# Optimization experiments

Measured on AMD Instinct MI355X. Metric: run time of the kernel, lower is better.

## Reference

```python
import jax, jax.numpy as jnp
import numpy as np

N_SIGMA = 1
K_MAX = 8          # max number of non-zero instance ids
FG_W = 1.0         # foreground_weight
W_INST, W_VAR, W_SEED = 1.0, 10.0, 1.0


def _lovasz_hinge_flat(logits, labels_f):
    # logits, labels_f: [P] flat; standard Lovasz hinge (descending-error sort)
    signs = 2.0 * labels_f - 1.0
    errors = 1.0 - logits * signs
    perm = jnp.argsort(-errors)
    errors_sorted = errors[perm]
    gt_sorted = labels_f[perm]
    gts = gt_sorted.sum()
    cum = jnp.cumsum(gt_sorted)
    intersection = gts - cum
    union = gts + jnp.cumsum(1.0 - gt_sorted)
    jaccard = 1.0 - intersection / union
    grad = jnp.concatenate([jaccard[:1], jaccard[1:] - jaccard[:-1]])
    return jnp.sum(jax.nn.relu(errors_sorted) * jax.lax.stop_gradient(grad))


def _spatial_emb_loss(prediction, instances, labels):
    B, C, H, W = prediction.shape
    inst = instances[:, 0]  # [B,H,W]
    # coordinate buffer: linspace over the full 1024x2048 grid, then sliced
    xm = jnp.linspace(0.0, 2.0, 2048)[:W]
    ym = jnp.linspace(0.0, 1.0, 1024)[:H]
    xym = jnp.stack([jnp.broadcast_to(xm[None, :], (H, W)),
                     jnp.broadcast_to(ym[:, None], (H, W))])  # [2,H,W]
    ids = jnp.arange(1, K_MAX + 1)

    def per_image(pred, ins, lab):
        spatial_emb = jnp.tanh(pred[0:2]) + xym            # [2,H,W]
        sigma = pred[2]                                     # [H,W] (n_sigma=1)
        seed = jax.nn.sigmoid(pred[3])                      # [H,W]
        bg = (lab == 0)
        seed_loss_bg = jnp.sum(jnp.where(bg, seed ** 2, 0.0))
        masks = (ins[None] == ids[:, None, None])           # [K,H,W]
        mf = masks.astype(pred.dtype)
        counts = mf.sum((1, 2))                             # [K]
        present = counts > 0
        cnt = jnp.maximum(counts, 1.0)
        # to_center=True: center = mean of xym over instance pixels
        center = jnp.einsum('chw,khw->kc', xym, mf) / cnt[:, None]   # [K,2]
        s_mean = jnp.einsum('hw,khw->k', sigma, mf) / cnt            # [K]
        var_k = jnp.einsum('khw,khw->k',
                           (sigma[None] - jax.lax.stop_gradient(s_mean)[:, None, None]) ** 2,
                           mf) / cnt
        s_exp = jnp.exp(10.0 * s_mean)                                # [K]
        d2 = jnp.sum((spatial_emb[None] - center[:, :, None, None]) ** 2, axis=1)  # [K,H,W]
        dist = jnp.exp(-s_exp[:, None, None] * d2)                    # [K,H,W]
        lov = jax.vmap(_lovasz_hinge_flat)(2.0 * dist.reshape(K_MAX, -1) - 1.0,
                                           mf.reshape(K_MAX, -1))     # [K]
        seed_fg = jnp.einsum('khw,khw->k',
                             (seed[None] - jax.lax.stop_gradient(dist)) ** 2, mf)
        objf = jnp.maximum(present.sum().astype(pred.dtype), 1.0)
        inst_loss = jnp.where(present, lov, 0.0).sum() / objf
        var_loss = jnp.where(present, var_k, 0.0).sum() / objf
        seed_loss = (seed_loss_bg + FG_W * jnp.where(present, seed_fg, 0.0).sum()) / (H * W)
        return W_INST * inst_loss + W_VAR * var_loss + W_SEED * seed_loss

    per = jax.vmap(per_image)(prediction, inst, labels)
    return per.mean() + 0.0 * prediction.sum()


def setup_inputs() -> dict:
    key = jax.random.key(0)
    k1, k2, k3 = jax.random.split(key, 3)
    B, H, W = 4, 512, 1024
    prediction = jax.random.normal(k1, (B, 2 + N_SIGMA + 1, H, W), dtype=jnp.float32)
    instances = jax.random.randint(k2, (B, 1, H, W), 0, K_MAX + 1, dtype=jnp.int32)
    labels = jax.random.randint(k3, (B, H, W), 0, 2, dtype=jnp.int32)
    return {"prediction": prediction, "instances": instances, "labels": labels}


def reference(prediction, instances, labels):
    return _spatial_emb_loss(prediction, instances, labels)
```

## Files before the change

kernel.cpp:

```cpp
#include <hip/hip_runtime.h>
#include <math.h>

namespace {
constexpr int B_ = 4, K_ = 8, W_ = 1024;
constexpr int N_ = 512 * 1024;
constexpr int M_ = 128;
constexpr int MP_ = M_ + 1;
constexpr int BK_ = B_ * K_;
constexpr int KM_ = K_ * M_;

constexpr int HB_ = 512;
constexpr int HBPB_ = HB_ / B_;
constexpr int HCH_ = N_ / HBPB_;
constexpr int SB_ = 1024;
constexpr int SBPB_ = SB_ / B_;
constexpr int SCH_ = N_ / SBPB_;
constexpr int NSTAT = 41;
constexpr int NHC_ = 4;

constexpr size_t GHN_OFF_W  = 0;
constexpr size_t GHF_OFF_W  = GHN_OFF_W + B_ * KM_;
constexpr size_t SFG_OFF_W  = GHF_OFF_W + B_ * KM_;
constexpr size_t PSTAT_OFF_W = SFG_OFF_W + (size_t)BK_ * HBPB_;
constexpr size_t WSF_OFF_W  = PSTAT_OFF_W + (size_t)B_ * NSTAT * SBPB_;

constexpr int CNT_OFF  = 0;
constexpr int OBJF_OFF = 32;
}

__device__ __forceinline__ float fsigmoid_(float x) { return 1.0f / (1.0f + __expf(-x)); }
__device__ __forceinline__ float ftanh_(float x) { return 1.0f - 2.0f / (__expf(2.0f * x) + 1.0f); }

__global__ __launch_bounds__(256) void stats_kernel(const float* __restrict__ pred,
                                                    const int* __restrict__ inst,
                                                    const int* __restrict__ lab,
                                                    float* __restrict__ pstat,
                                                    unsigned int* __restrict__ gh,
                                                    float* __restrict__ out) {
    int tid = threadIdx.x;
    if (blockIdx.x < 32) {
        gh[blockIdx.x * 256 + tid] = 0u;
        if (blockIdx.x == 0 && tid == 0) out[0] = 0.0f;
    }
    int b = blockIdx.x >> 8;
    int blk = blockIdx.x & (SBPB_ - 1);
    int pix0 = blk * SCH_;

    const float* sigp = pred + ((long long)b * 4 + 2) * N_;
    const float* p3p  = pred + ((long long)b * 4 + 3) * N_;
    const int*   insp = inst + (long long)b * N_;
    const int*   labp = lab  + (long long)b * N_;

    float acc[NSTAT];
#pragma unroll
    for (int i = 0; i < NSTAT; i++) acc[i] = 0.0f;

#pragma unroll
    for (int it = 0; it < SCH_ / (256 * 4); it++) {
        int base = pix0 + (it * 256 + tid) * 4;
        float4 sg = *(const float4*)(sigp + base);
        float4 q3 = *(const float4*)(p3p + base);
        int4 in4 = *(const int4*)(insp + base);
        int4 lb4 = *(const int4*)(labp + base);
        float ss[4] = {sg.x, sg.y, sg.z, sg.w};
        float qq[4] = {q3.x, q3.y, q3.z, q3.w};
        int ii[4] = {in4.x, in4.y, in4.z, in4.w};
        int ll[4] = {lb4.x, lb4.y, lb4.z, lb4.w};
#pragma unroll
        for (int j = 0; j < 4; j++) {
            int pix = base + j;
            float xm = (float)(pix & (W_ - 1)) * (2.0f / 2047.0f);
            float ym = (float)(pix >> 10) * (1.0f / 1023.0f);
            float seed = fsigmoid_(qq[j]);
            if (ll[j] == 0) acc[40] += seed * seed;
            float s = ss[j];
#pragma unroll
            for (int k = 0; k < K_; k++) {
                float m = (ii[j] == k + 1) ? 1.0f : 0.0f;
                acc[k * 5]     += m;
                acc[k * 5 + 1] += m * xm;
                acc[k * 5 + 2] += m * ym;
                acc[k * 5 + 3] += m * s;
                acc[k * 5 + 4] += m * s * s;
            }
        }
    }
#pragma unroll
    for (int i = 0; i < NSTAT; i++) {
        float v = acc[i];
#pragma unroll
        for (int off = 32; off; off >>= 1) v += __shfl_down(v, off, 64);
        acc[i] = v;
    }
    __shared__ float xw[4][NSTAT];
    if ((tid & 63) == 0) {
        int w = tid >> 6;
#pragma unroll
        for (int i = 0; i < NSTAT; i++) xw[w][i] = acc[i];
    }
    __syncthreads();
    if (tid < NSTAT)
        pstat[((b * NSTAT + tid) << 8) + blk] =
            xw[0][tid] + xw[1][tid] + xw[2][tid] + xw[3][tid];
}

__global__ __launch_bounds__(256) void hist_kernel(const float* __restrict__ pred,
                                                   const int* __restrict__ inst,
                                                   const float* __restrict__ pstat,
                                                   float* __restrict__ wsf,
                                                   unsigned int* __restrict__ ghn,
                                                   unsigned int* __restrict__ ghf,
                                                   float* __restrict__ sfgpart,
                                                   float* __restrict__ out) {
    __shared__ float sq[NSTAT][4];
    __shared__ float ssum[NSTAT];
    __shared__ float prm[K_][4];
    __shared__ float svar[K_];
    __shared__ int spres[K_];
    __shared__ unsigned int hsh[NHC_][K_ * MP_];
    __shared__ float xfg[4][K_];

    int tid = threadIdx.x;
    int b = blockIdx.x >> 7;
    int blk = blockIdx.x & (HBPB_ - 1);
    int pix0 = blk * HCH_;

    if (tid < NSTAT * 4) {
        int row = tid >> 2, q = tid & 3;
        const float4* p = (const float4*)(pstat + ((size_t)(b * NSTAT + row) << 8)) + q * 16;
        float4 a = {0, 0, 0, 0};
#pragma unroll
        for (int j = 0; j < 16; j++) {
            float4 v = p[j];
            a.x += v.x; a.y += v.y; a.z += v.z; a.w += v.w;
        }
        sq[row][q] = (a.x + a.y) + (a.z + a.w);
    }
    for (int i = tid; i < NHC_ * K_ * MP_; i += 256) (&hsh[0][0])[i] = 0u;
    __syncthreads();
    if (tid < NSTAT) ssum[tid] = (sq[tid][0] + sq[tid][1]) + (sq[tid][2] + sq[tid][3]);
    __syncthreads();
    if (tid < K_) {
        float counts = ssum[tid * 5];
        float cnt = fmaxf(counts, 1.0f);
        float smean = ssum[tid * 5 + 3] / cnt;
        prm[tid][0] = ssum[tid * 5 + 1] / cnt;
        prm[tid][1] = ssum[tid * 5 + 2] / cnt;
        prm[tid][2] = expf(10.0f * smean);
        prm[tid][3] = counts;
        if (blk == 0) {
            svar[tid] = (counts > 0.0f) ? ssum[tid * 5 + 4] / cnt - smean * smean : 0.0f;
            spres[tid] = counts > 0.0f ? 1 : 0;
            wsf[CNT_OFF + b * K_ + tid] = counts;
        }
    }
    __syncthreads();
    if (blk == 0 && tid == 0) {
        float np = 0.0f, vl = 0.0f;
#pragma unroll
        for (int k = 0; k < K_; k++) { np += (float)spres[k]; vl += svar[k]; }
        float objf = fmaxf(np, 1.0f);
        wsf[OBJF_OFF + b] = objf;
        atomicAdd(out, (10.0f * vl / objf + ssum[40] / (float)N_) * (1.0f / (float)B_));
    }

    float cx[K_], cy[K_], sxp[K_];
    bool prs[K_];
#pragma unroll
    for (int k = 0; k < K_; k++) {
        cx[k] = prm[k][0]; cy[k] = prm[k][1]; sxp[k] = prm[k][2];
        prs[k] = prm[k][3] > 0.0f;
    }
    unsigned int* hpriv = &hsh[tid & 3][0];

    const float* p0p = pred + ((long long)b * 4) * N_;
    const float* p1p = p0p + N_;
    const float* p3p = p0p + 3LL * N_;
    const int* insp = inst + (long long)b * N_;

    float sfg[K_];
#pragma unroll
    for (int k = 0; k < K_; k++) sfg[k] = 0.0f;

#pragma unroll
    for (int it = 0; it < HCH_ / (256 * 4); it++) {
        int base = pix0 + (it * 256 + tid) * 4;
        float4 a0 = *(const float4*)(p0p + base);
        float4 a1 = *(const float4*)(p1p + base);
        float4 a3 = *(const float4*)(p3p + base);
        int4 in4 = *(const int4*)(insp + base);
        float v0[4] = {a0.x, a0.y, a0.z, a0.w};
        float v1[4] = {a1.x, a1.y, a1.z, a1.w};
        float v3[4] = {a3.x, a3.y, a3.z, a3.w};
        int ii[4] = {in4.x, in4.y, in4.z, in4.w};
#pragma unroll
        for (int j = 0; j < 4; j++) {
            int pix = base + j;
            float sex = ftanh_(v0[j]) + (float)(pix & (W_ - 1)) * (2.0f / 2047.0f);
            float sey = ftanh_(v1[j]) + (float)(pix >> 10) * (1.0f / 1023.0f);
            float seed = fsigmoid_(v3[j]);
            int ins = ii[j];
#pragma unroll
            for (int k = 0; k < K_; k++) {
                if (prs[k]) {
                    float dx = sex - cx[k];
                    float dy = sey - cy[k];
                    float dist = __expf(-sxp[k] * (dx * dx + dy * dy));
                    bool fg = (ins == k + 1);
                    int ib = (int)fminf(128.0f * dist, 127.0f);
                    int bin = fg ? 127 - ib : ib;
                    atomicAdd(hpriv + (k * MP_ + bin), fg ? 0x10001u : 1u);
                    if (fg) { float d = seed - dist; sfg[k] += d * d; }
                }
            }
        }
    }
    __syncthreads();

    for (int i = tid; i < KM_; i += 256) {
        int r = (i >> 7) * MP_ + (i & (M_ - 1));
        unsigned int s = hsh[0][r] + hsh[1][r] + hsh[2][r] + hsh[3][r];
        if (s) {
            atomicAdd(&ghn[b * KM_ + i], s & 0xffffu);
            unsigned int hi = s >> 16;
            if (hi) atomicAdd(&ghf[b * KM_ + i], hi);
        }
    }

#pragma unroll
    for (int k = 0; k < K_; k++) {
        float v = sfg[k];
#pragma unroll
        for (int off = 32; off; off >>= 1) v += __shfl_down(v, off, 64);
        sfg[k] = v;
    }
    if ((tid & 63) == 0) {
        int w = tid >> 6;
#pragma unroll
        for (int k = 0; k < K_; k++) xfg[w][k] = sfg[k];
    }
    __syncthreads();
    if (tid < K_)
        sfgpart[(size_t)(b * K_ + tid) * HBPB_ + blk] =
            xfg[0][tid] + xfg[1][tid] + xfg[2][tid] + xfg[3][tid];
}

__global__ __launch_bounds__(256) void lovasz_kernel(const unsigned int* __restrict__ ghn,
                                                     const unsigned int* __restrict__ ghf,
                                                     const float* __restrict__ sfgpart,
                                                     const float* __restrict__ wsf,
                                                     float* __restrict__ out) {
    int bk = blockIdx.x;
    int b = bk >> 3, k = bk & 7;
    int tid = threadIdx.x;

    __shared__ unsigned int sn[M_], sf[M_];
    __shared__ float lovp;
    __shared__ float xs[2];
    if (tid < M_) {
        sn[tid] = ghn[(size_t)b * KM_ + k * M_ + tid];
        sf[tid] = ghf[(size_t)b * KM_ + k * M_ + tid];
    }
    __syncthreads();

    float pcnt = wsf[CNT_OFF + bk];
    float pp = fmaxf(pcnt, 1.0f);

    if (tid < 64) {
        uint2 vn = *(const uint2*)&sn[2 * tid];
        uint2 vf = *(const uint2*)&sf[2 * tid];
        unsigned long long p0 = ((unsigned long long)vn.x << 32) | (unsigned long long)vf.x;
        unsigned long long p1 = ((unsigned long long)vn.y << 32) | (unsigned long long)vf.y;
        unsigned long long T = p0 + p1;
#pragma unroll
        for (int off = 1; off < 64; off <<= 1) {
            unsigned long long t = __shfl_down(T, off, 64);
            if (tid + off < 64) T += t;
        }
        unsigned long long S0 = T;
        unsigned long long S1 = T - p0;
        float acc;
        {
            unsigned int R = (unsigned int)(S0 >> 32), F = (unsigned int)S0;
            float J = (R == 0) ? 0.0f : (1.0f - (pp - (float)F) / (pp + (float)(R - F)));
            acc = (tid == 0 ? 0.5f : 1.0f) * J;
        }
        {
            unsigned int R = (unsigned int)(S1 >> 32), F = (unsigned int)S1;
            float J = (R == 0) ? 0.0f : (1.0f - (pp - (float)F) / (pp + (float)(R - F)));
            acc += J;
        }
#pragma unroll
        for (int off = 32; off; off >>= 1) acc += __shfl_down(acc, off, 64);
        if (tid == 0) lovp = acc;
    } else if (tid >= 128) {
        float sv = sfgpart[(size_t)bk * HBPB_ + (tid - 128)];
#pragma unroll
        for (int off = 32; off; off >>= 1) sv += __shfl_down(sv, off, 64);
        if ((tid & 63) == 0) xs[(tid - 128) >> 6] = sv;
    }
    __syncthreads();

    if (tid == 0 && pcnt > 0.0f) {
        float lov = lovp * (2.0f / (float)M_);
        float sfgt = xs[0] + xs[1];
        float objf = wsf[OBJF_OFF + b];
        atomicAdd(out, (lov / objf + sfgt / (float)N_) * (1.0f / (float)B_));
    }
}

extern "C" void kernel_launch(void* const* d_in, const int* in_sizes, int n_in,
                              void* d_out, int out_size, void* d_ws, size_t ws_size,
                              hipStream_t stream) {
    const float* pred = (const float*)d_in[0];
    const int* inst = (const int*)d_in[1];
    const int* lab = (const int*)d_in[2];
    float* out = (float*)d_out;

    unsigned int* gh = (unsigned int*)d_ws;
    unsigned int* ghn = gh + GHN_OFF_W;
    unsigned int* ghf = gh + GHF_OFF_W;
    float* sfgpart = (float*)d_ws + SFG_OFF_W;
    float* pstat = (float*)d_ws + PSTAT_OFF_W;
    float* wsf = (float*)d_ws + WSF_OFF_W;

    stats_kernel<<<SB_, 256, 0, stream>>>(pred, inst, lab, pstat, gh, out);
    hist_kernel<<<HB_, 256, 0, stream>>>(pred, inst, pstat, wsf, ghn, ghf, sfgpart, out);
    lovasz_kernel<<<BK_, 256, 0, stream>>>(ghn, ghf, sfgpart, wsf, out);
}
```

Baseline: 117.4 us.

## Fuse Lovasz finalization into histogram kernel via last-block ticket counter

Removes the separate lovasz_kernel launch by having the last hist block per image (detected with an atomic ticket counter) compute the Lovasz and seed-foreground terms. Partial sums are written atomically and read back with agent-scope atomic loads so the last block sees other blocks' histogram updates. This saves one kernel launch and its gap, at the cost of a serialized tail in one block per image and relying on relaxed-atomic visibility ordering.

```diff
diff --git a/kernel.cpp b/kernel.cpp
--- a/kernel.cpp
+++ b/kernel.cpp
@@ -20,12 +20,9 @@
 
 constexpr size_t GHN_OFF_W  = 0;
 constexpr size_t GHF_OFF_W  = GHN_OFF_W + B_ * KM_;
-constexpr size_t SFG_OFF_W  = GHF_OFF_W + B_ * KM_;
-constexpr size_t PSTAT_OFF_W = SFG_OFF_W + (size_t)BK_ * HBPB_;
-constexpr size_t WSF_OFF_W  = PSTAT_OFF_W + (size_t)B_ * NSTAT * SBPB_;
-
-constexpr int CNT_OFF  = 0;
-constexpr int OBJF_OFF = 32;
+constexpr size_t SFGS_OFF_W = GHF_OFF_W + B_ * KM_;
+constexpr size_t CTR_OFF_W  = SFGS_OFF_W + (size_t)BK_ * HBPB_;
+constexpr size_t PSTAT_OFF_W = CTR_OFF_W + 8;
 }
 
 __device__ __forceinline__ float fsigmoid_(float x) { return 1.0f / (1.0f + __expf(-x)); }
@@ -36,11 +33,14 @@
                                                     const int* __restrict__ lab,
                                                     float* __restrict__ pstat,
                                                     unsigned int* __restrict__ gh,
+                                                    unsigned int* __restrict__ ctr,
                                                     float* __restrict__ out) {
     int tid = threadIdx.x;
     if (blockIdx.x < 32) {
         gh[blockIdx.x * 256 + tid] = 0u;
         if (blockIdx.x == 0 && tid == 0) out[0] = 0.0f;
+    } else if (blockIdx.x == 32 && tid < 8) {
+        ctr[tid] = 0u;
     }
     int b = blockIdx.x >> 8;
     int blk = blockIdx.x & (SBPB_ - 1);
@@ -107,10 +107,10 @@
 __global__ __launch_bounds__(256) void hist_kernel(const float* __restrict__ pred,
                                                    const int* __restrict__ inst,
                                                    const float* __restrict__ pstat,
-                                                   float* __restrict__ wsf,
                                                    unsigned int* __restrict__ ghn,
                                                    unsigned int* __restrict__ ghf,
-                                                   float* __restrict__ sfgpart,
+                                                   float* __restrict__ sfgs,
+                                                   unsigned int* __restrict__ ctr,
                                                    float* __restrict__ out) {
     __shared__ float sq[NSTAT][4];
     __shared__ float ssum[NSTAT];
@@ -119,6 +119,7 @@
     __shared__ int spres[K_];
     __shared__ unsigned int hsh[NHC_][K_ * MP_];
     __shared__ float xfg[4][K_];
+    __shared__ unsigned int stkt;
 
     int tid = threadIdx.x;
     int b = blockIdx.x >> 7;
@@ -151,7 +152,6 @@
         if (blk == 0) {
             svar[tid] = (counts > 0.0f) ? ssum[tid * 5 + 4] / cnt - smean * smean : 0.0f;
             spres[tid] = counts > 0.0f ? 1 : 0;
-            wsf[CNT_OFF + b * K_ + tid] = counts;
         }
     }
     __syncthreads();
@@ -160,7 +160,6 @@
 #pragma unroll
         for (int k = 0; k < K_; k++) { np += (float)spres[k]; vl += svar[k]; }
         float objf = fmaxf(np, 1.0f);
-        wsf[OBJF_OFF + b] = objf;
         atomicAdd(out, (10.0f * vl / objf + ssum[40] / (float)N_) * (1.0f / (float)B_));
     }
 
@@ -241,41 +240,38 @@
     }
     __syncthreads();
     if (tid < K_)
-        sfgpart[(size_t)(b * K_ + tid) * HBPB_ + blk] =
-            xfg[0][tid] + xfg[1][tid] + xfg[2][tid] + xfg[3][tid];
-}
-
-__global__ __launch_bounds__(256) void lovasz_kernel(const unsigned int* __restrict__ ghn,
-                                                     const unsigned int* __restrict__ ghf,
-                                                     const float* __restrict__ sfgpart,
-                                                     const float* __restrict__ wsf,
-                                                     float* __restrict__ out) {
-    int bk = blockIdx.x;
-    int b = bk >> 3, k = bk & 7;
-    int tid = threadIdx.x;
-
-    __shared__ unsigned int sn[M_], sf[M_];
-    __shared__ float lovp;
-    __shared__ float xs[2];
-    if (tid < M_) {
-        sn[tid] = ghn[(size_t)b * KM_ + k * M_ + tid];
-        sf[tid] = ghf[(size_t)b * KM_ + k * M_ + tid];
-    }
-    __syncthreads();
-
-    float pcnt = wsf[CNT_OFF + bk];
-    float pp = fmaxf(pcnt, 1.0f);
-
-    if (tid < 64) {
-        uint2 vn = *(const uint2*)&sn[2 * tid];
-        uint2 vf = *(const uint2*)&sf[2 * tid];
-        unsigned long long p0 = ((unsigned long long)vn.x << 32) | (unsigned long long)vf.x;
-        unsigned long long p1 = ((unsigned long long)vn.y << 32) | (unsigned long long)vf.y;
+        atomicExch(&sfgs[(size_t)(b * K_ + tid) * HBPB_ + blk],
+                   (xfg[0][tid] + xfg[1][tid]) + (xfg[2][tid] + xfg[3][tid]));
+
+    __syncthreads();
+    if (tid == 0) stkt = atomicAdd(&ctr[b], 1u);
+    __syncthreads();
+    if (stkt != (unsigned int)(HBPB_ - 1)) return;
+
+    int wv = tid >> 6, ln = tid & 63;
+    float np = 0.0f;
+#pragma unroll
+    for (int j = 0; j < K_; j++) np += (prm[j][3] > 0.0f) ? 1.0f : 0.0f;
+    float objf = fmaxf(np, 1.0f);
+
+    for (int kk = 0; kk < 2; kk++) {
+        int k = wv * 2 + kk;
+        float pcnt = prm[k][3];
+        if (pcnt <= 0.0f) continue;
+        float pp = fmaxf(pcnt, 1.0f);
+
+        size_t gb = (size_t)b * KM_ + (size_t)k * M_;
+        unsigned int n0 = __hip_atomic_load(&ghn[gb + 2 * ln],     __ATOMIC_RELAXED, __HIP_MEMORY_SCOPE_AGENT);
+        unsigned int n1 = __hip_atomic_load(&ghn[gb + 2 * ln + 1], __ATOMIC_RELAXED, __HIP_MEMORY_SCOPE_AGENT);
+        unsigned int f0 = __hip_atomic_load(&ghf[gb + 2 * ln],     __ATOMIC_RELAXED, __HIP_MEMORY_SCOPE_AGENT);
+        unsigned int f1 = __hip_atomic_load(&ghf[gb + 2 * ln + 1], __ATOMIC_RELAXED, __HIP_MEMORY_SCOPE_AGENT);
+        unsigned long long p0 = ((unsigned long long)n0 << 32) | (unsigned long long)f0;
+        unsigned long long p1 = ((unsigned long long)n1 << 32) | (unsigned long long)f1;
         unsigned long long T = p0 + p1;
 #pragma unroll
         for (int off = 1; off < 64; off <<= 1) {
             unsigned long long t = __shfl_down(T, off, 64);
-            if (tid + off < 64) T += t;
+            if (ln + off < 64) T += t;
         }
         unsigned long long S0 = T;
         unsigned long long S1 = T - p0;
@@ -283,29 +279,27 @@
         {
             unsigned int R = (unsigned int)(S0 >> 32), F = (unsigned int)S0;
             float J = (R == 0) ? 0.0f : (1.0f - (pp - (float)F) / (pp + (float)(R - F)));
-            acc = (tid == 0 ? 0.5f : 1.0f) * J;
+            acc = (ln == 0 ? 0.5f : 1.0f) * J;
         }
         {
             unsigned int R = (unsigned int)(S1 >> 32), F = (unsigned int)S1;
             float J = (R == 0) ? 0.0f : (1.0f - (pp - (float)F) / (pp + (float)(R - F)));
             acc += J;
         }
-#pragma unroll
-        for (int off = 32; off; off >>= 1) acc += __shfl_down(acc, off, 64);
-        if (tid == 0) lovp = acc;
-    } else if (tid >= 128) {
-        float sv = sfgpart[(size_t)bk * HBPB_ + (tid - 128)];
-#pragma unroll
-        for (int off = 32; off; off >>= 1) sv += __shfl_down(sv, off, 64);
-        if ((tid & 63) == 0) xs[(tid - 128) >> 6] = sv;
-    }
-    __syncthreads();
-
-    if (tid == 0 && pcnt > 0.0f) {
-        float lov = lovp * (2.0f / (float)M_);
-        float sfgt = xs[0] + xs[1];
-        float objf = wsf[OBJF_OFF + b];
-        atomicAdd(out, (lov / objf + sfgt / (float)N_) * (1.0f / (float)B_));
+        const float* sp = sfgs + (size_t)(b * K_ + k) * HBPB_;
+        float sa = __hip_atomic_load(&sp[ln],      __ATOMIC_RELAXED, __HIP_MEMORY_SCOPE_AGENT);
+        float sb = __hip_atomic_load(&sp[64 + ln], __ATOMIC_RELAXED, __HIP_MEMORY_SCOPE_AGENT);
+#pragma unroll
+        for (int off = 32; off; off >>= 1) {
+            acc += __shfl_down(acc, off, 64);
+            sa  += __shfl_down(sa, off, 64);
+            sb  += __shfl_down(sb, off, 64);
+        }
+        if (ln == 0) {
+            float lov = acc * (2.0f / (float)M_);
+            float sfgt = sa + sb;
+            atomicAdd(out, (lov / objf + sfgt / (float)N_) * (1.0f / (float)B_));
+        }
     }
 }
 
@@ -320,11 +314,10 @@
     unsigned int* gh = (unsigned int*)d_ws;
     unsigned int* ghn = gh + GHN_OFF_W;
     unsigned int* ghf = gh + GHF_OFF_W;
-    float* sfgpart = (float*)d_ws + SFG_OFF_W;
+    float* sfgs = (float*)d_ws + SFGS_OFF_W;
+    unsigned int* ctr = (unsigned int*)d_ws + CTR_OFF_W;
     float* pstat = (float*)d_ws + PSTAT_OFF_W;
-    float* wsf = (float*)d_ws + WSF_OFF_W;
-
-    stats_kernel<<<SB_, 256, 0, stream>>>(pred, inst, lab, pstat, gh, out);
-    hist_kernel<<<HB_, 256, 0, stream>>>(pred, inst, pstat, wsf, ghn, ghf, sfgpart, out);
-    lovasz_kernel<<<BK_, 256, 0, stream>>>(ghn, ghf, sfgpart, wsf, out);
+
+    stats_kernel<<<SB_, 256, 0, stream>>>(pred, inst, lab, pstat, gh, ctr, out);
+    hist_kernel<<<HB_, 256, 0, stream>>>(pred, inst, pstat, ghn, ghf, sfgs, ctr, out);
 }
```

Result: no change. 119.1 us (+1.4%).
